# Optimization experiments

Measured on AMD Instinct MI355X. Metric: run time of the kernel, lower is better.

The kernel has to match this reference:

```python
import jax, jax.numpy as jnp
import numpy as np

B, L, D, H, NF = 4, 2048, 1024, 16, 32
THRESHOLD = 0.1


def setup_inputs() -> dict:
    key = jax.random.key(0)
    ks = jax.random.split(key, 12)
    s = 1.0 / np.sqrt(D)
    return {
        "q_x": jax.random.normal(ks[0], (B, L, D), jnp.float32),
        "k_x": jax.random.normal(ks[1], (B, L, D), jnp.float32),
        "v_x": jax.random.normal(ks[2], (B, L, D), jnp.float32),
        "energy_coeffs": jax.random.normal(ks[3], (B, L, NF), jnp.float32),
        "Wq": jax.random.normal(ks[4], (D, D), jnp.float32) * s,
        "bq": jnp.zeros((D,), jnp.float32),
        "Wk": jax.random.normal(ks[5], (D, D), jnp.float32) * s,
        "bk": jnp.zeros((D,), jnp.float32),
        "Wv": jax.random.normal(ks[6], (D, D), jnp.float32) * s,
        "bv": jnp.zeros((D,), jnp.float32),
        "Wo": jax.random.normal(ks[7], (D, D), jnp.float32) * s,
        "bo": jnp.zeros((D,), jnp.float32),
    }


def reference(q_x, k_x, v_x, energy_coeffs, Wq, bq, Wk, bk, Wv, bv, Wo, bo):
    Bq, Lq, Dm = q_x.shape
    Dh = Dm // H
    # projections, split heads: [B, H, L, Dh]
    Q = (q_x @ Wq + bq).reshape(Bq, Lq, H, Dh).transpose(0, 2, 1, 3)
    K = (k_x @ Wk + bk).reshape(Bq, -1, H, Dh).transpose(0, 2, 1, 3)
    V = (v_x @ Wv + bv).reshape(Bq, -1, H, Dh).transpose(0, 2, 1, 3)
    scores = jnp.einsum("bhqd,bhkd->bhqk", Q, K) / jnp.sqrt(jnp.float32(Dh))
    # frequency-energy gate per key
    energy = jnp.abs(energy_coeffs).mean(axis=-1)                  # [B, Lk]
    energy = energy / (energy.max(axis=-1, keepdims=True) + 1e-8)
    gate = (energy > THRESHOLD).astype(scores.dtype) * 0.9 + 0.1   # [B, Lk]
    scores = scores * gate[:, None, None, :]
    attn = jax.nn.softmax(scores, axis=-1)
    attn = jnp.nan_to_num(attn, nan=0.0)
    out = jnp.einsum("bhqk,bhkd->bhqd", attn, V)
    out = out.transpose(0, 2, 1, 3).reshape(Bq, Lq, Dm)
    return out @ Wo + bo
```

## Files before the change

### kernel.cpp

```cpp
#include <hip/hip_runtime.h>

typedef unsigned short u16;
typedef unsigned int u32;
typedef __attribute__((ext_vector_type(4))) float fx4;
typedef __attribute__((ext_vector_type(16))) float fx16;
typedef __attribute__((ext_vector_type(4))) u32 ux4;
typedef __attribute__((ext_vector_type(4))) u16 hx4;
typedef __attribute__((ext_vector_type(8))) short sx8;

#define B_ 4
#define L_ 2048
#define D_ 1024
#define H_ 16
#define DH_ 64
#define M_ 8192
#define QSCALE 0.18033688011112042f

__device__ __forceinline__ u16 f2bf(float f) {
  u32 u = __float_as_uint(f);
  return (u16)((u + 0x7FFFu + ((u >> 16) & 1u)) >> 16);
}

__device__ __forceinline__ void gl_lds16(const void* g, void* l) {
  __builtin_amdgcn_global_load_lds((const __attribute__((address_space(1))) void*)g,
                                   (__attribute__((address_space(3))) void*)l, 16, 0, 0);
}

__device__ __forceinline__ u32 cvtpk_bf(float lo, float hi) {
  u32 r;
  asm("v_cvt_pk_bf16_f32 %0, %1, %2" : "=v"(r) : "v"(lo), "v"(hi));
  return r;
}

__global__ __launch_bounds__(256) void wt_kernel(const float* __restrict__ Wq, const float* __restrict__ Wk,
                                                 const float* __restrict__ Wv, const float* __restrict__ Wo,
                                                 u16* __restrict__ Wt0) {
  const float* W = blockIdx.z == 0 ? Wq : (blockIdx.z == 1 ? Wk : (blockIdx.z == 2 ? Wv : Wo));
  u16* Wt = Wt0 + (size_t)blockIdx.z * D_ * D_;
  __shared__ float t[32][33];
  const int n0 = blockIdx.x * 32, k0 = blockIdx.y * 32;
  const int tx = threadIdx.x & 31, ty = threadIdx.x >> 5;
#pragma unroll
  for (int r = 0; r < 32; r += 8) t[ty + r][tx] = W[(size_t)(k0 + ty + r) * D_ + n0 + tx];
  __syncthreads();
#pragma unroll
  for (int r = 0; r < 32; r += 8) Wt[(size_t)(n0 + ty + r) * D_ + k0 + tx] = f2bf(t[tx][ty + r]);
}

__global__ __launch_bounds__(256) void energy_kernel(const float* __restrict__ ec, float* __restrict__ energy,
                                                     u32* __restrict__ emax) {
  const int i = blockIdx.x * 256 + threadIdx.x;
  const fx4* p = (const fx4*)(ec + (size_t)i * 32);
  float s = 0.f;
#pragma unroll
  for (int j = 0; j < 8; j++) {
    fx4 v = p[j];
    s += fabsf(v[0]) + fabsf(v[1]) + fabsf(v[2]) + fabsf(v[3]);
  }
  const float e = s * (1.0f / 32.0f);
  energy[i] = e;
  float m = e;
#pragma unroll
  for (int d = 1; d < 64; d <<= 1) m = fmaxf(m, __shfl_xor(m, d));
  if ((threadIdx.x & 63) == 0) atomicMax(emax + (i >> 11), __float_as_uint(m));
}

__global__ __launch_bounds__(256) void gate_kernel(const float* __restrict__ energy, const u32* __restrict__ emax,
                                                   float* __restrict__ gate) {
  const int i = blockIdx.x * 256 + threadIdx.x;
  const float m = __uint_as_float(emax[i >> 11]);
  gate[i] = (energy[i] / (m + 1e-8f) > 0.1f) ? 1.0f : 0.1f;
}

template <int MODE>
__global__ __launch_bounds__(256) void gemm_kernel(const float* __restrict__ A0, const float* __restrict__ A1,
                                                   const float* __restrict__ A2, const u16* __restrict__ Abf,
                                                   const u16* __restrict__ Wtall, const float* __restrict__ bq,
                                                   const float* __restrict__ bk, const float* __restrict__ bv,
                                                   const float* __restrict__ bo, const float* __restrict__ gate,
                                                   u16* __restrict__ Qo, u16* __restrict__ Ko,
                                                   u16* __restrict__ Vo, float* __restrict__ out) {
  __shared__ u16 Al[2][128][40];
  __shared__ u16 Bl[2][128][40];

  const int z = blockIdx.z;
  const float* Af = nullptr;
  const float* bias;
  const u16* Wt;
  float scale = 1.0f;
  if (MODE == 0) {
    Af = (z == 0) ? A0 : (z == 1 ? A1 : A2);
    bias = (z == 0) ? bq : (z == 1 ? bk : bv);
    Wt = Wtall + (size_t)z * (D_ * D_);
    if (z == 0) scale = QSCALE;
  } else {
    bias = bo;
    Wt = Wtall + (size_t)3 * (D_ * D_);
  }
  const int m0 = blockIdx.x * 128, n0 = blockIdx.y * 128;
  const int tid = threadIdx.x, w = tid >> 6, lane = tid & 63;
  const int cc = lane & 15, g = lane >> 4;
  const int wm = w >> 1, wn = w & 1;

  fx4 acc[4][4];
#pragma unroll
  for (int i = 0; i < 4; i++)
#pragma unroll
    for (int j = 0; j < 4; j++) acc[i][j] = (fx4){0.f, 0.f, 0.f, 0.f};

  fx4 areg[4];
  ux4 aregb[2];
  ux4 breg[2];
  const int ar = tid >> 3, ac = (tid & 7) * 4;
  const int br = tid >> 2, bc = (tid & 3) * 8;

  auto loadT = [&](int kt) {
    if (MODE == 0) {
#pragma unroll
      for (int r = 0; r < 4; r++)
        areg[r] = *(const fx4*)(Af + (size_t)(m0 + ar + r * 32) * D_ + kt * 32 + ac);
    } else {
#pragma unroll
      for (int r = 0; r < 2; r++)
        aregb[r] = *(const ux4*)(Abf + (size_t)(m0 + br + r * 64) * D_ + kt * 32 + bc);
    }
#pragma unroll
    for (int r = 0; r < 2; r++)
      breg[r] = *(const ux4*)(Wt + (size_t)(n0 + br + r * 64) * D_ + kt * 32 + bc);
  };

  auto writeT = [&](int bf) {
    if (MODE == 0) {
#pragma unroll
      for (int r = 0; r < 4; r++) {
        hx4 hv;
#pragma unroll
        for (int i = 0; i < 4; i++) hv[i] = f2bf(areg[r][i]);
        *(hx4*)&Al[bf][ar + r * 32][ac] = hv;
      }
    } else {
#pragma unroll
      for (int r = 0; r < 2; r++) *(ux4*)&Al[bf][br + r * 64][bc] = aregb[r];
    }
#pragma unroll
    for (int r = 0; r < 2; r++) *(ux4*)&Bl[bf][br + r * 64][bc] = breg[r];
  };

  auto comp = [&](int bf) {
    sx8 a[4], bb[4];
#pragma unroll
    for (int mf = 0; mf < 4; mf++) a[mf] = *(const sx8*)&Al[bf][wm * 64 + mf * 16 + cc][g * 8];
#pragma unroll
    for (int nf = 0; nf < 4; nf++) bb[nf] = *(const sx8*)&Bl[bf][wn * 64 + nf * 16 + cc][g * 8];
#pragma unroll
    for (int mf = 0; mf < 4; mf++)
#pragma unroll
      for (int nf = 0; nf < 4; nf++)
        acc[mf][nf] = __builtin_amdgcn_mfma_f32_16x16x32_bf16(a[mf], bb[nf], acc[mf][nf], 0, 0, 0);
  };

  loadT(0);
  writeT(0);
  __syncthreads();
#pragma unroll 1
  for (int kt = 0; kt < 32; kt += 2) {
    loadT(kt + 1);
    comp(0);
    writeT(1);
    __syncthreads();
    if (kt + 2 < 32) loadT(kt + 2);
    comp(1);
    if (kt + 2 < 32) writeT(0);
    __syncthreads();
  }

#pragma unroll
  for (int mf = 0; mf < 4; mf++) {
    const int mbase = m0 + wm * 64 + mf * 16 + g * 4;
#pragma unroll
    for (int nf = 0; nf < 4; nf++) {
      const int n = n0 + wn * 64 + nf * 16 + cc;
      const float bs = bias[n];
      if (MODE == 1) {
#pragma unroll
        for (int i = 0; i < 4; i++) out[(size_t)(mbase + i) * D_ + n] = acc[mf][nf][i] + bs;
      } else if (z == 2) {
        const int b = mbase >> 11, l = mbase & 2047;
        const int h = n >> 6, dh = n & 63;
        hx4 hv;
#pragma unroll
        for (int i = 0; i < 4; i++) hv[i] = f2bf(acc[mf][nf][i] + bs);
        *(hx4*)(Vo + ((size_t)(b * H_ + h) * DH_ + dh) * L_ + l) = hv;
      } else {
        u16* dst = (z == 0) ? Qo : Ko;
        const int h = n >> 6, dh = n & 63;
#pragma unroll
        for (int i = 0; i < 4; i++) {
          const int m = mbase + i, b = m >> 11, l = m & 2047;
          float val = (acc[mf][nf][i] + bs) * scale;
          if (z == 1) val *= gate[m];
          dst[((size_t)(b * H_ + h) * L_ + l) * DH_ + dh] = f2bf(val);
        }
      }
    }
  }
}

__global__ __launch_bounds__(256) void attn_kernel(const u16* __restrict__ Q, const u16* __restrict__ K,
                                                   const u16* __restrict__ Vt, u16* __restrict__ O) {
  __shared__ __align__(16) u16 Kl[2][4096];
  __shared__ __align__(16) u16 Vl[2][4096];

  const int bh = blockIdx.y, b = bh >> 4, h = bh & 15;
  const int q0 = blockIdx.x * 128;
  const char* Kb = (const char*)(K + (size_t)bh * (L_ * DH_));
  const char* Vb = (const char*)(Vt + (size_t)bh * (DH_ * L_));
  const u16* Qb = Q + (size_t)bh * (L_ * DH_);

  const int tid = threadIdx.x, w = tid >> 6, lane = tid & 63;
  const int l31 = lane & 31, half = lane >> 5;

  sx8 qf[4];
  const u16* qrow = Qb + (size_t)(q0 + w * 32 + l31) * DH_;
#pragma unroll
  for (int ks = 0; ks < 4; ks++) qf[ks] = *(const sx8*)(qrow + ks * 16 + half * 8);

  fx16 oa0, oa1;
#pragma unroll
  for (int r = 0; r < 16; r++) {
    oa0[r] = 0.f;
    oa1[r] = 0.f;
  }
  float m = -3.0e38f, lsum = 0.f;

  int koff[2], voff[2];
#pragma unroll
  for (int j = 0; j < 2; j++) {
    const int c = w * 2 + j, sub = c >> 2, ks = c & 3;
    koff[j] = (sub * 32 + l31) * 128 + ks * 32 + half * 16;
    voff[j] = (sub * 32 + l31) * 4096 + ks * 32 + half * 16;
  }

  auto stage = [&](int t, int bf) {
#pragma unroll
    for (int j = 0; j < 2; j++) {
      const int c = w * 2 + j;
      gl_lds16(Kb + (size_t)t * 8192 + koff[j], (char*)&Kl[bf][0] + c * 1024);
      gl_lds16(Vb + (size_t)t * 128 + voff[j], (char*)&Vl[bf][0] + c * 1024);
    }
  };

  auto tile = [&](int bf) {
    const u16* KL = &Kl[bf][0];
    const u16* VL = &Vl[bf][0];
    fx16 SA, SB;
#pragma unroll
    for (int r = 0; r < 16; r++) {
      SA[r] = 0.f;
      SB[r] = 0.f;
    }
    __builtin_amdgcn_s_setprio(1);
#pragma unroll
    for (int ks = 0; ks < 4; ks++) {
      sx8 k0 = *(const sx8*)(KL + ks * 512 + lane * 8);
      sx8 k1 = *(const sx8*)(KL + (4 + ks) * 512 + lane * 8);
      SA = __builtin_amdgcn_mfma_f32_32x32x16_bf16(k0, qf[ks], SA, 0, 0, 0);
      SB = __builtin_amdgcn_mfma_f32_32x32x16_bf16(k1, qf[ks], SB, 0, 0, 0);
    }
    __builtin_amdgcn_s_setprio(0);

    fx16 mm;
#pragma unroll
    for (int r = 0; r < 16; r++) mm[r] = fmaxf(SA[r], SB[r]);
#pragma unroll
    for (int r = 0; r < 8; r++) mm[r] = fmaxf(mm[r], mm[r + 8]);
#pragma unroll
    for (int r = 0; r < 4; r++) mm[r] = fmaxf(mm[r], mm[r + 4]);
    float pm = fmaxf(fmaxf(mm[0], mm[1]), fmaxf(mm[2], mm[3]));
    pm = fmaxf(pm, __shfl_xor(pm, 32));
    if (!__all(pm - m <= 8.0f)) {
      const float mn = fmaxf(m, pm);
      const float sf = exp2f(m - mn);
      m = mn;
      lsum *= sf;
      oa0 *= sf;
      oa1 *= sf;
    }
    float rs = 0.f;
#pragma unroll
    for (int r = 0; r < 16; r++) {
      SA[r] = exp2f(SA[r] - m);
      SB[r] = exp2f(SB[r] - m);
      rs += SA[r] + SB[r];
    }
    lsum += rs;

    sx8 pb[4];
#define MKPB(S, base, dst)                                 \
  {                                                        \
    u32 A0 = cvtpk_bf((S)[(base) + 0], (S)[(base) + 1]);   \
    u32 A1 = cvtpk_bf((S)[(base) + 2], (S)[(base) + 3]);   \
    u32 A2 = cvtpk_bf((S)[(base) + 4], (S)[(base) + 5]);   \
    u32 A3 = cvtpk_bf((S)[(base) + 6], (S)[(base) + 7]);   \
    asm("v_permlane32_swap_b32 %0, %1" : "+v"(A0), "+v"(A2)); \
    asm("v_permlane32_swap_b32 %0, %1" : "+v"(A1), "+v"(A3)); \
    ux4 wv = {A0, A1, A2, A3};                             \
    dst = __builtin_bit_cast(sx8, wv);                     \
  }
    MKPB(SA, 0, pb[0]);
    MKPB(SA, 8, pb[1]);
    MKPB(SB, 0, pb[2]);
    MKPB(SB, 8, pb[3]);
#undef MKPB

    __builtin_amdgcn_s_setprio(1);
#pragma unroll
    for (int ks = 0; ks < 4; ks++) {
      sx8 v0 = *(const sx8*)(VL + ks * 512 + lane * 8);
      sx8 v1 = *(const sx8*)(VL + (4 + ks) * 512 + lane * 8);
      oa0 = __builtin_amdgcn_mfma_f32_32x32x16_bf16(v0, pb[ks], oa0, 0, 0, 0);
      oa1 = __builtin_amdgcn_mfma_f32_32x32x16_bf16(v1, pb[ks], oa1, 0, 0, 0);
    }
    __builtin_amdgcn_s_setprio(0);
  };

  stage(0, 0);
#pragma unroll 1
  for (int t = 0; t < 32; t += 2) {
    __syncthreads();
    stage(t + 1, 1);
    tile(0);
    __syncthreads();
    if (t + 2 < 32) stage(t + 2, 0);
    tile(1);
  }

  const float linv = 1.0f / (lsum + __shfl_xor(lsum, 32));
  u16* orow = O + ((size_t)b * L_ + q0 + w * 32 + l31) * D_ + h * DH_;
#pragma unroll
  for (int r = 0; r < 16; r++) {
    const int d = (r & 3) + 8 * (r >> 2) + 4 * half;
    orow[d] = f2bf(oa0[r] * linv);
    orow[32 + d] = f2bf(oa1[r] * linv);
  }
}

extern "C" void kernel_launch(void* const* d_in, const int* in_sizes, int n_in, void* d_out, int out_size,
                              void* d_ws, size_t ws_size, hipStream_t stream) {
  const float* q_x = (const float*)d_in[0];
  const float* k_x = (const float*)d_in[1];
  const float* v_x = (const float*)d_in[2];
  const float* ec = (const float*)d_in[3];
  const float* Wq = (const float*)d_in[4];
  const float* bq = (const float*)d_in[5];
  const float* Wk = (const float*)d_in[6];
  const float* bk = (const float*)d_in[7];
  const float* Wv = (const float*)d_in[8];
  const float* bv = (const float*)d_in[9];
  const float* Wo = (const float*)d_in[10];
  const float* bo = (const float*)d_in[11];
  float* out = (float*)d_out;

  char* ws = (char*)d_ws;
  u16* Wt = (u16*)ws;
  u16* Qws = (u16*)(ws + (size_t)(8u << 20));
  u16* Kws = (u16*)(ws + (size_t)(24u << 20));
  u16* Vtws = (u16*)(ws + (size_t)(40u << 20));
  u16* Ows = (u16*)(ws + (size_t)(56u << 20));
  float* energy = (float*)(ws + (size_t)(72u << 20));
  float* gate = energy + M_;
  u32* emax = (u32*)(gate + M_);

  hipMemsetAsync(emax, 0, 4 * sizeof(u32), stream);
  wt_kernel<<<dim3(32, 32, 4), 256, 0, stream>>>(Wq, Wk, Wv, Wo, Wt);
  energy_kernel<<<dim3(M_ / 256), 256, 0, stream>>>(ec, energy, emax);
  gate_kernel<<<dim3(M_ / 256), 256, 0, stream>>>(energy, emax, gate);
  gemm_kernel<0><<<dim3(64, 8, 3), 256, 0, stream>>>(q_x, k_x, v_x, nullptr, Wt, bq, bk, bv, bo, gate, Qws,
                                                     Kws, Vtws, out);
  attn_kernel<<<dim3(16, 64), 256, 0, stream>>>(Qws, Kws, Vtws, Ows);
  gemm_kernel<1><<<dim3(64, 8, 1), 256, 0, stream>>>(nullptr, nullptr, nullptr, Ows, Wt, bq, bk, bv, bo, gate,
                                                     Qws, Kws, Vtws, out);
}
```

Measured before the change: 441.8 us.

## Stage GEMM tiles via direct global-to-LDS loads with swizzle and pre-cast inputs

Replaces the register-staged global→LDS copies in the projection GEMMs with global_load_lds async transfers into an XOR-swizzled LDS layout. When the workspace is large enough, a separate kernel first converts q/k/v from fp32 to bf16 so the QKV GEMM can use the same async path. Q and K are also stored in row-major [B,L,D] order, and the attention kernel's addressing is updated to match. This trades an extra pass over the inputs, plus workspace use, for less register pressure and better load/compute overlap in the GEMM.

```diff
diff --git a/kernel.cpp b/kernel.cpp
--- a/kernel.cpp
+++ b/kernel.cpp
@@ -47,6 +47,22 @@
   for (int r = 0; r < 32; r += 8) Wt[(size_t)(n0 + ty + r) * D_ + k0 + tx] = f2bf(t[tx][ty + r]);
 }
 
+__global__ __launch_bounds__(256) void xcast_kernel(const float* __restrict__ q, const float* __restrict__ k,
+                                                    const float* __restrict__ v, u16* __restrict__ out) {
+  const u32 i = blockIdx.x * 256 + threadIdx.x;
+  const u32 sel = i >> 20;
+  const size_t off = (size_t)(i & 0xFFFFFu) * 8;
+  const float* src = sel == 0 ? q : (sel == 1 ? k : v);
+  fx4 a = *(const fx4*)(src + off);
+  fx4 b = *(const fx4*)(src + off + 4);
+  ux4 o;
+  o[0] = cvtpk_bf(a[0], a[1]);
+  o[1] = cvtpk_bf(a[2], a[3]);
+  o[2] = cvtpk_bf(b[0], b[1]);
+  o[3] = cvtpk_bf(b[2], b[3]);
+  *(ux4*)(out + (size_t)i * 8) = o;
+}
+
 __global__ __launch_bounds__(256) void energy_kernel(const float* __restrict__ ec, float* __restrict__ energy,
                                                      u32* __restrict__ emax) {
   const int i = blockIdx.x * 256 + threadIdx.x;
@@ -72,35 +88,32 @@
   gate[i] = (energy[i] / (m + 1e-8f) > 0.1f) ? 1.0f : 0.1f;
 }
 
-template <int MODE>
-__global__ __launch_bounds__(256) void gemm_kernel(const float* __restrict__ A0, const float* __restrict__ A1,
-                                                   const float* __restrict__ A2, const u16* __restrict__ Abf,
+template <int OUTM, int AF32>
+__global__ __launch_bounds__(256) void gemm_kernel(const u16* __restrict__ Abf, const float* __restrict__ A0,
+                                                   const float* __restrict__ A1, const float* __restrict__ A2,
                                                    const u16* __restrict__ Wtall, const float* __restrict__ bq,
                                                    const float* __restrict__ bk, const float* __restrict__ bv,
                                                    const float* __restrict__ bo, const float* __restrict__ gate,
                                                    u16* __restrict__ Qo, u16* __restrict__ Ko,
                                                    u16* __restrict__ Vo, float* __restrict__ out) {
-  __shared__ u16 Al[2][128][40];
-  __shared__ u16 Bl[2][128][40];
-
-  const int z = blockIdx.z;
+  __shared__ __align__(16) u16 Asm[AF32 ? 10240 : 8192];
+  __shared__ __align__(16) u16 Bsm[8192];
+
+  const int z = (OUTM == 0) ? blockIdx.z : 3;
+  const float* bias = (OUTM == 1) ? bo : (z == 0 ? bq : (z == 1 ? bk : bv));
+  const u16* Wt = Wtall + (size_t)z * (D_ * D_);
   const float* Af = nullptr;
-  const float* bias;
-  const u16* Wt;
-  float scale = 1.0f;
-  if (MODE == 0) {
+  const u16* Ab = nullptr;
+  if constexpr (AF32)
     Af = (z == 0) ? A0 : (z == 1 ? A1 : A2);
-    bias = (z == 0) ? bq : (z == 1 ? bk : bv);
-    Wt = Wtall + (size_t)z * (D_ * D_);
-    if (z == 0) scale = QSCALE;
-  } else {
-    bias = bo;
-    Wt = Wtall + (size_t)3 * (D_ * D_);
-  }
+  else
+    Ab = (OUTM == 0) ? Abf + (size_t)z * ((size_t)M_ * D_) : Abf;
+
   const int m0 = blockIdx.x * 128, n0 = blockIdx.y * 128;
   const int tid = threadIdx.x, w = tid >> 6, lane = tid & 63;
   const int cc = lane & 15, g = lane >> 4;
   const int wm = w >> 1, wn = w & 1;
+  const int fsw = (cc >> 1) & 3;
 
   fx4 acc[4][4];
 #pragma unroll
@@ -108,50 +121,61 @@
 #pragma unroll
     for (int j = 0; j < 4; j++) acc[i][j] = (fx4){0.f, 0.f, 0.f, 0.f};
 
+  const int srow = tid >> 2;
+  const int scsw = (tid & 3) ^ ((srow >> 1) & 3);
+  const char* Bs0 = (const char*)(Wt + (size_t)(n0 + srow) * D_) + scsw * 16;
+  const char* Bs1 = (const char*)(Wt + (size_t)(n0 + 64 + srow) * D_) + scsw * 16;
+  const char* As0 = nullptr;
+  const char* As1 = nullptr;
+  if constexpr (!AF32) {
+    As0 = (const char*)(Ab + (size_t)(m0 + srow) * D_) + scsw * 16;
+    As1 = (const char*)(Ab + (size_t)(m0 + 64 + srow) * D_) + scsw * 16;
+  }
+
   fx4 areg[4];
-  ux4 aregb[2];
-  ux4 breg[2];
   const int ar = tid >> 3, ac = (tid & 7) * 4;
-  const int br = tid >> 2, bc = (tid & 3) * 8;
-
-  auto loadT = [&](int kt) {
-    if (MODE == 0) {
+
+  auto prefetch = [&](int kt, int bf) {
+    const int ko = kt * 64;
+    gl_lds16(Bs0 + ko, (char*)Bsm + bf * 8192 + w * 1024);
+    gl_lds16(Bs1 + ko, (char*)Bsm + bf * 8192 + 4096 + w * 1024);
+    if constexpr (!AF32) {
+      gl_lds16(As0 + ko, (char*)Asm + bf * 8192 + w * 1024);
+      gl_lds16(As1 + ko, (char*)Asm + bf * 8192 + 4096 + w * 1024);
+    } else {
 #pragma unroll
       for (int r = 0; r < 4; r++)
         areg[r] = *(const fx4*)(Af + (size_t)(m0 + ar + r * 32) * D_ + kt * 32 + ac);
-    } else {
-#pragma unroll
-      for (int r = 0; r < 2; r++)
-        aregb[r] = *(const ux4*)(Abf + (size_t)(m0 + br + r * 64) * D_ + kt * 32 + bc);
-    }
-#pragma unroll
-    for (int r = 0; r < 2; r++)
-      breg[r] = *(const ux4*)(Wt + (size_t)(n0 + br + r * 64) * D_ + kt * 32 + bc);
+    }
   };
 
-  auto writeT = [&](int bf) {
-    if (MODE == 0) {
+  auto commitA = [&](int bf) {
+    if constexpr (AF32) {
 #pragma unroll
       for (int r = 0; r < 4; r++) {
         hx4 hv;
 #pragma unroll
         for (int i = 0; i < 4; i++) hv[i] = f2bf(areg[r][i]);
-        *(hx4*)&Al[bf][ar + r * 32][ac] = hv;
+        *(hx4*)&Asm[bf * 5120 + (ar + r * 32) * 40 + ac] = hv;
       }
-    } else {
-#pragma unroll
-      for (int r = 0; r < 2; r++) *(ux4*)&Al[bf][br + r * 64][bc] = aregb[r];
-    }
-#pragma unroll
-    for (int r = 0; r < 2; r++) *(ux4*)&Bl[bf][br + r * 64][bc] = breg[r];
+    }
   };
 
   auto comp = [&](int bf) {
     sx8 a[4], bb[4];
 #pragma unroll
-    for (int mf = 0; mf < 4; mf++) a[mf] = *(const sx8*)&Al[bf][wm * 64 + mf * 16 + cc][g * 8];
-#pragma unroll
-    for (int nf = 0; nf < 4; nf++) bb[nf] = *(const sx8*)&Bl[bf][wn * 64 + nf * 16 + cc][g * 8];
+    for (int mf = 0; mf < 4; mf++) {
+      const int r = wm * 64 + mf * 16 + cc;
+      if constexpr (AF32)
+        a[mf] = *(const sx8*)&Asm[bf * 5120 + r * 40 + g * 8];
+      else
+        a[mf] = *(const sx8*)((const char*)Asm + bf * 8192 + r * 64 + ((g ^ fsw) * 16));
+    }
+#pragma unroll
+    for (int nf = 0; nf < 4; nf++) {
+      const int r = wn * 64 + nf * 16 + cc;
+      bb[nf] = *(const sx8*)((const char*)Bsm + bf * 8192 + r * 64 + ((g ^ fsw) * 16));
+    }
 #pragma unroll
     for (int mf = 0; mf < 4; mf++)
 #pragma unroll
@@ -159,18 +183,18 @@
         acc[mf][nf] = __builtin_amdgcn_mfma_f32_16x16x32_bf16(a[mf], bb[nf], acc[mf][nf], 0, 0, 0);
   };
 
-  loadT(0);
-  writeT(0);
+  prefetch(0, 0);
+  commitA(0);
   __syncthreads();
 #pragma unroll 1
   for (int kt = 0; kt < 32; kt += 2) {
-    loadT(kt + 1);
+    prefetch(kt + 1, 1);
     comp(0);
-    writeT(1);
+    commitA(1);
     __syncthreads();
-    if (kt + 2 < 32) loadT(kt + 2);
+    if (kt + 2 < 32) prefetch(kt + 2, 0);
     comp(1);
-    if (kt + 2 < 32) writeT(0);
+    if (kt + 2 < 32) commitA(0);
     __syncthreads();
   }
 
@@ -181,25 +205,26 @@
     for (int nf = 0; nf < 4; nf++) {
       const int n = n0 + wn * 64 + nf * 16 + cc;
       const float bs = bias[n];
-      if (MODE == 1) {
+      if constexpr (OUTM == 1) {
 #pragma unroll
         for (int i = 0; i < 4; i++) out[(size_t)(mbase + i) * D_ + n] = acc[mf][nf][i] + bs;
-      } else if (z == 2) {
-        const int b = mbase >> 11, l = mbase & 2047;
-        const int h = n >> 6, dh = n & 63;
-        hx4 hv;
-#pragma unroll
-        for (int i = 0; i < 4; i++) hv[i] = f2bf(acc[mf][nf][i] + bs);
-        *(hx4*)(Vo + ((size_t)(b * H_ + h) * DH_ + dh) * L_ + l) = hv;
       } else {
-        u16* dst = (z == 0) ? Qo : Ko;
-        const int h = n >> 6, dh = n & 63;
-#pragma unroll
-        for (int i = 0; i < 4; i++) {
-          const int m = mbase + i, b = m >> 11, l = m & 2047;
-          float val = (acc[mf][nf][i] + bs) * scale;
-          if (z == 1) val *= gate[m];
-          dst[((size_t)(b * H_ + h) * L_ + l) * DH_ + dh] = f2bf(val);
+        if (z == 2) {
+          const int b = mbase >> 11, l = mbase & 2047;
+          const int h = n >> 6, dh = n & 63;
+          hx4 hv;
+#pragma unroll
+          for (int i = 0; i < 4; i++) hv[i] = f2bf(acc[mf][nf][i] + bs);
+          *(hx4*)(Vo + ((size_t)(b * H_ + h) * DH_ + dh) * L_ + l) = hv;
+        } else {
+          u16* dst = (z == 0) ? Qo : Ko;
+#pragma unroll
+          for (int i = 0; i < 4; i++) {
+            const int m = mbase + i;
+            float val = acc[mf][nf][i] + bs;
+            val = (z == 0) ? val * QSCALE : val * gate[m];
+            dst[(size_t)m * D_ + n] = f2bf(val);
+          }
         }
       }
     }
@@ -213,15 +238,15 @@
 
   const int bh = blockIdx.y, b = bh >> 4, h = bh & 15;
   const int q0 = blockIdx.x * 128;
-  const char* Kb = (const char*)(K + (size_t)bh * (L_ * DH_));
+  const char* Kb = (const char*)K + ((size_t)b * L_ * D_ + h * DH_) * 2;
   const char* Vb = (const char*)(Vt + (size_t)bh * (DH_ * L_));
-  const u16* Qb = Q + (size_t)bh * (L_ * DH_);
+  const u16* Qb = Q + (size_t)b * L_ * D_ + h * DH_;
 
   const int tid = threadIdx.x, w = tid >> 6, lane = tid & 63;
   const int l31 = lane & 31, half = lane >> 5;
 
   sx8 qf[4];
-  const u16* qrow = Qb + (size_t)(q0 + w * 32 + l31) * DH_;
+  const u16* qrow = Qb + (size_t)(q0 + w * 32 + l31) * D_;
 #pragma unroll
   for (int ks = 0; ks < 4; ks++) qf[ks] = *(const sx8*)(qrow + ks * 16 + half * 8);
 
@@ -237,7 +262,7 @@
 #pragma unroll
   for (int j = 0; j < 2; j++) {
     const int c = w * 2 + j, sub = c >> 2, ks = c & 3;
-    koff[j] = (sub * 32 + l31) * 128 + ks * 32 + half * 16;
+    koff[j] = (sub * 32 + l31) * 2048 + ks * 32 + half * 16;
     voff[j] = (sub * 32 + l31) * 4096 + ks * 32 + half * 16;
   }
 
@@ -245,7 +270,7 @@
 #pragma unroll
     for (int j = 0; j < 2; j++) {
       const int c = w * 2 + j;
-      gl_lds16(Kb + (size_t)t * 8192 + koff[j], (char*)&Kl[bf][0] + c * 1024);
+      gl_lds16(Kb + (size_t)t * (64 * D_ * 2) + koff[j], (char*)&Kl[bf][0] + c * 1024);
       gl_lds16(Vb + (size_t)t * 128 + voff[j], (char*)&Vl[bf][0] + c * 1024);
     }
   };
@@ -362,12 +387,15 @@
   float* out = (float*)d_out;
 
   char* ws = (char*)d_ws;
+  const bool big = ws_size >= ((size_t)105 << 20);
   u16* Wt = (u16*)ws;
   u16* Qws = (u16*)(ws + (size_t)(8u << 20));
   u16* Kws = (u16*)(ws + (size_t)(24u << 20));
   u16* Vtws = (u16*)(ws + (size_t)(40u << 20));
+  u16* Xb = (u16*)(ws + (size_t)(56u << 20));
   u16* Ows = (u16*)(ws + (size_t)(56u << 20));
-  float* energy = (float*)(ws + (size_t)(72u << 20));
+  char* stats = ws + ((size_t)(big ? 104u : 72u) << 20);
+  float* energy = (float*)stats;
   float* gate = energy + M_;
   u32* emax = (u32*)(gate + M_);
 
@@ -375,9 +403,15 @@
   wt_kernel<<<dim3(32, 32, 4), 256, 0, stream>>>(Wq, Wk, Wv, Wo, Wt);
   energy_kernel<<<dim3(M_ / 256), 256, 0, stream>>>(ec, energy, emax);
   gate_kernel<<<dim3(M_ / 256), 256, 0, stream>>>(energy, emax, gate);
-  gemm_kernel<0><<<dim3(64, 8, 3), 256, 0, stream>>>(q_x, k_x, v_x, nullptr, Wt, bq, bk, bv, bo, gate, Qws,
-                                                     Kws, Vtws, out);
+  if (big) {
+    xcast_kernel<<<dim3(3 * M_ * (D_ / 8) / 256), 256, 0, stream>>>(q_x, k_x, v_x, Xb);
+    gemm_kernel<0, 0><<<dim3(64, 8, 3), 256, 0, stream>>>(Xb, nullptr, nullptr, nullptr, Wt, bq, bk, bv, bo,
+                                                          gate, Qws, Kws, Vtws, out);
+  } else {
+    gemm_kernel<0, 1><<<dim3(64, 8, 3), 256, 0, stream>>>(nullptr, q_x, k_x, v_x, Wt, bq, bk, bv, bo, gate,
+                                                          Qws, Kws, Vtws, out);
+  }
   attn_kernel<<<dim3(16, 64), 256, 0, stream>>>(Qws, Kws, Vtws, Ows);
-  gemm_kernel<1><<<dim3(64, 8, 1), 256, 0, stream>>>(nullptr, nullptr, nullptr, Ows, Wt, bq, bk, bv, bo, gate,
-                                                     Qws, Kws, Vtws, out);
-}
+  gemm_kernel<1, 0><<<dim3(64, 8, 1), 256, 0, stream>>>(Ows, nullptr, nullptr, nullptr, Wt, bq, bk, bv, bo,
+                                                        gate, Qws, Kws, Vtws, out);
+}
```

Measured after the change: 434.3 us. Within noise of the previous version (-1.7%).
